# Kernel optimization log

Measured on AMD Instinct MI355X. Metric: run time of the kernel, lower is better.

The kernel has to match this reference:

```python
import jax, jax.numpy as jnp
import numpy as np

N, E, G = 50000, 800000, 512
F_IN, ED, NUM_CLASSES = 128, 3, 10
H1, C1, C2 = 4, 32, 64


def _add_self_loops(src, dst, eattr, n):
    # PyG add_self_loops with fill_value='mean': loop attr = mean of incoming edge attrs
    cnt = jax.ops.segment_sum(jnp.ones_like(dst, dtype=eattr.dtype), dst, num_segments=n)
    loop = jax.ops.segment_sum(eattr, dst, num_segments=n) / jnp.maximum(cnt, 1.0)[:, None]
    ar = jnp.arange(n)
    return (jnp.concatenate([src, ar]), jnp.concatenate([dst, ar]),
            jnp.concatenate([eattr, loop], axis=0))


def _gatv2(x, src, dst, eattr, Wl, bl, Wr, br, We, att, bias, heads, out_ch, concat, n):
    xl = (x @ Wl.T + bl).reshape(n, heads, out_ch)   # source transform (lin_l)
    xr = (x @ Wr.T + br).reshape(n, heads, out_ch)   # target transform (lin_r)
    ee = (eattr @ We.T).reshape(-1, heads, out_ch)   # edge transform (lin_edge, no bias)
    m = jax.nn.leaky_relu(xl[src] + xr[dst] + ee, 0.2)  # [E', H, C]
    score = jnp.einsum('ehc,hc->eh', m, att)
    # segment softmax over incoming edges of each target node
    smax = jax.ops.segment_max(score, dst, num_segments=n)
    ex = jnp.exp(score - smax[dst])
    denom = jax.ops.segment_sum(ex, dst, num_segments=n)
    alpha = ex / denom[dst]
    out = jax.ops.segment_sum(alpha[:, :, None] * xl[src], dst, num_segments=n)
    out = out.reshape(n, heads * out_ch) if concat else out.mean(axis=1)
    return out + bias


def setup_inputs() -> dict:
    key = jax.random.key(0)
    ks = jax.random.split(key, 24)
    s = 0.1
    return {
        'x': jax.random.normal(ks[0], (N, F_IN), jnp.float32),
        'edge_index': jax.random.randint(ks[1], (2, E), 0, N),
        'edge_attr': jax.random.normal(ks[2], (E, ED), jnp.float32),
        'batch': jnp.sort(jax.random.randint(ks[3], (N,), 0, G)),
        'u': jax.random.normal(ks[4], (G, 1), jnp.float32),
        'Wl1': jax.random.normal(ks[5], (H1 * C1, F_IN), jnp.float32) * s,
        'bl1': jnp.zeros((H1 * C1,), jnp.float32),
        'Wr1': jax.random.normal(ks[6], (H1 * C1, F_IN), jnp.float32) * s,
        'br1': jnp.zeros((H1 * C1,), jnp.float32),
        'We1': jax.random.normal(ks[7], (H1 * C1, ED), jnp.float32) * s,
        'att1': jax.random.normal(ks[8], (H1, C1), jnp.float32) * s,
        'b1': jnp.zeros((H1 * C1,), jnp.float32),
        'Wl2': jax.random.normal(ks[9], (C2, H1 * C1), jnp.float32) * s,
        'bl2': jnp.zeros((C2,), jnp.float32),
        'Wr2': jax.random.normal(ks[10], (C2, H1 * C1), jnp.float32) * s,
        'br2': jnp.zeros((C2,), jnp.float32),
        'We2': jax.random.normal(ks[11], (C2, ED), jnp.float32) * s,
        'att2': jax.random.normal(ks[12], (1, C2), jnp.float32) * s,
        'b2': jnp.zeros((C2,), jnp.float32),
        'W_lin1': jax.random.normal(ks[13], (32, 65), jnp.float32) * s,
        'b_lin1': jnp.zeros((32,), jnp.float32),
        'W_head': jax.random.normal(ks[14], (NUM_CLASSES, 32), jnp.float32) * s,
        'b_head': jnp.zeros((NUM_CLASSES,), jnp.float32),
    }


def reference(x, edge_index, edge_attr, batch, u,
              Wl1, bl1, Wr1, br1, We1, att1, b1,
              Wl2, bl2, Wr2, br2, We2, att2, b2,
              W_lin1, b_lin1, W_head, b_head):
    n = x.shape[0]
    src, dst, ea = _add_self_loops(edge_index[0], edge_index[1], edge_attr, n)
    h = jax.nn.elu(_gatv2(x, src, dst, ea, Wl1, bl1, Wr1, br1, We1, att1, b1, H1, C1, True, n))
    h = jax.nn.elu(_gatv2(h, src, dst, ea, Wl2, bl2, Wr2, br2, We2, att2, b2, 1, C2, False, n))
    cnt = jax.ops.segment_sum(jnp.ones((n,), h.dtype), batch, num_segments=G)
    pooled = jax.ops.segment_sum(h, batch, num_segments=G) / jnp.maximum(cnt, 1.0)[:, None]
    z = jax.nn.relu(jnp.concatenate([pooled, u], axis=1) @ W_lin1.T + b_lin1)
    return z @ W_head.T + b_head
```

## Files before the change

### kernel.cpp

```cpp
#include <hip/hip_runtime.h>
#include <hip/hip_fp16.h>
#include <math.h>


union H2U { __half2 h; unsigned u; };
typedef _Float16 hv2_t __attribute__((ext_vector_type(2)));
typedef unsigned uv4_t __attribute__((ext_vector_type(4)));

__device__ __forceinline__ __half2 hmax2(__half2 a, __half2 b) {
  union { __half2 h; hv2_t v; } x, y, r;
  x.h = a; y.h = b;
  r.v = __builtin_elementwise_max(x.v, y.v);
  return r.h;
}

#if __has_builtin(__builtin_amdgcn_fdot2)
__device__ __forceinline__ float dot2f(__half2 a, __half2 b, float c) {
  union { __half2 h; hv2_t v; } x, y;
  x.h = a; y.h = b;
  return __builtin_amdgcn_fdot2(x.v, y.v, c, false);
}
#else
__device__ __forceinline__ float dot2f(__half2 a, __half2 b, float c) {
  float2 af = __half22float2(a), bf = __half22float2(b);
  return fmaf(af.x, bf.x, fmaf(af.y, bf.y, c));
}
#endif

__global__ void hist_k(const int* __restrict__ dst, int* __restrict__ deg, int E) {
  int e = blockIdx.x * 256 + threadIdx.x;
  if (e < E) atomicAdd(&deg[dst[e]], 1);
}

__global__ void blocksum_k(const int* __restrict__ deg, int* __restrict__ bsum, int N) {
  __shared__ int s[256];
  int i = blockIdx.x * 256 + threadIdx.x;
  s[threadIdx.x] = (i < N) ? deg[i] : 0;
  __syncthreads();
  for (int off = 128; off; off >>= 1) {
    if (threadIdx.x < off) s[threadIdx.x] += s[threadIdx.x + off];
    __syncthreads();
  }
  if (threadIdx.x == 0) bsum[blockIdx.x] = s[0];
}

__global__ void scan_bsum_k(int* __restrict__ bsum, int nb) {
  __shared__ int s[256];
  int t = threadIdx.x;
  s[t] = (t < nb) ? bsum[t] : 0;
  __syncthreads();
  for (int off = 1; off < 256; off <<= 1) {
    int v = (t >= off) ? s[t - off] : 0;
    __syncthreads();
    if (t >= off) s[t] += v;
    __syncthreads();
  }
  int excl = (t == 0) ? 0 : s[t - 1];
  if (t < nb) bsum[t] = excl;
}

__global__ void writeptr_k(const int* __restrict__ deg, const int* __restrict__ bsum,
                           int* __restrict__ rowptr, int* __restrict__ cursor, int N, int E) {
  __shared__ int s[256];
  int t = threadIdx.x;
  int i = blockIdx.x * 256 + t;
  s[t] = (i < N) ? deg[i] : 0;
  __syncthreads();
  for (int off = 1; off < 256; off <<= 1) {
    int v = (t >= off) ? s[t - off] : 0;
    __syncthreads();
    if (t >= off) s[t] += v;
    __syncthreads();
  }
  int excl = bsum[blockIdx.x] + ((t == 0) ? 0 : s[t - 1]);
  if (i < N) {
    rowptr[i] = excl;
    cursor[i] = excl;
  }
  if (i == N - 1) rowptr[N] = E;
}

__global__ void fill_k(const int* __restrict__ src, const int* __restrict__ dst,
                       const float* __restrict__ eattr, int* __restrict__ cursor,
                       uint4* __restrict__ erec, int E) {
  int e = blockIdx.x * 256 + threadIdx.x;
  if (e >= E) return;
  int d = dst[e];
  int pos = atomicAdd(&cursor[d], 1);
  H2U a0, a1, a2;
  float e0 = eattr[e * 3 + 0], e1 = eattr[e * 3 + 1], e2 = eattr[e * 3 + 2];
  a0.h = __floats2half2_rn(e0, e0);
  a1.h = __floats2half2_rn(e1, e1);
  a2.h = __floats2half2_rn(e2, e2);
  uv4_t v = {(unsigned)src[e], a0.u, a1.u, a2.u};
  __builtin_nontemporal_store(v, (uv4_t*)&erec[pos]);
}

template <int J>
__global__ __launch_bounds__(256, 3) void node_linear2t_k(
    const float* __restrict__ X,
    const float* __restrict__ W1, const float* __restrict__ b1v,
    const float* __restrict__ W2, const float* __restrict__ b2v,
    __half* __restrict__ out1, float* __restrict__ out2, int nrows) {
  constexpr int K = 128, KB = 32;
  constexpr int JG = J / 4;
  constexpr int RG = 256 / JG;
  constexpr int RB = RG * 4;
  constexpr int XP2 = RB + 4;
  constexpr int WP2 = J + 4;
  __shared__ __align__(16) __half2 sXT2[K / 2][XP2];
  __shared__ __align__(16) __half2 sW1T2[KB / 2][WP2];
  __shared__ __align__(16) __half2 sW2T2[KB / 2][WP2];

  int tid = threadIdx.x;
  int n0 = blockIdx.x * RB;

  {
    int r = tid & (RB - 1);
    int kq0 = tid / RB;
    constexpr int KQS = 256 / RB;
    int n = n0 + r;
    bool ok = n < nrows;
    for (int kq = kq0; kq < K / 4; kq += KQS) {
      float4 v = ok ? *(const float4*)&X[(size_t)n * K + kq * 4]
                    : make_float4(0.f, 0.f, 0.f, 0.f);
      sXT2[kq * 2 + 0][r] = __floats2half2_rn(v.x, v.y);
      sXT2[kq * 2 + 1][r] = __floats2half2_rn(v.z, v.w);
    }
  }

  int jg = tid % JG;
  int rg = tid / JG;
  float acc1[4][4] = {}, acc2[4][4] = {};

  for (int kb = 0; kb < K / KB; ++kb) {
    __syncthreads();
    {
      int j = tid & (J - 1);
      int kq0 = tid / J;
      constexpr int KQS = 256 / J;
      for (int kq = kq0; kq < KB / 4; kq += KQS) {
        float4 v1 = *(const float4*)&W1[(size_t)j * K + kb * KB + kq * 4];
        float4 v2 = *(const float4*)&W2[(size_t)j * K + kb * KB + kq * 4];
        sW1T2[kq * 2 + 0][j] = __floats2half2_rn(v1.x, v1.y);
        sW1T2[kq * 2 + 1][j] = __floats2half2_rn(v1.z, v1.w);
        sW2T2[kq * 2 + 0][j] = __floats2half2_rn(v2.x, v2.y);
        sW2T2[kq * 2 + 1][j] = __floats2half2_rn(v2.z, v2.w);
      }
    }
    __syncthreads();
#pragma unroll
    for (int k2 = 0; k2 < KB / 2; ++k2) {
      const __half2* xp = &sXT2[kb * (KB / 2) + k2][rg * 4];
      const __half2* w1p = &sW1T2[k2][jg * 4];
      const __half2* w2p = &sW2T2[k2][jg * 4];
      __half2 xs2[4], w1s2[4], w2s2[4];
      *(float4*)xs2 = *(const float4*)xp;
      *(float4*)w1s2 = *(const float4*)w1p;
      *(float4*)w2s2 = *(const float4*)w2p;
#pragma unroll
      for (int i = 0; i < 4; ++i)
#pragma unroll
        for (int q = 0; q < 4; ++q) {
          acc1[i][q] = dot2f(xs2[i], w1s2[q], acc1[i][q]);
          acc2[i][q] = dot2f(xs2[i], w2s2[q], acc2[i][q]);
        }
    }
  }

  float4 bv1 = *(const float4*)&b1v[jg * 4];
  float4 bv2 = *(const float4*)&b2v[jg * 4];
#pragma unroll
  for (int i = 0; i < 4; ++i) {
    int n = n0 + rg * 4 + i;
    if (n < nrows) {
      H2U a, b;
      a.h = __floats2half2_rn(acc1[i][0] + bv1.x, acc1[i][1] + bv1.y);
      b.h = __floats2half2_rn(acc1[i][2] + bv1.z, acc1[i][3] + bv1.w);
      *(uint2*)&out1[(size_t)n * J + jg * 4] = make_uint2(a.u, b.u);
      float4 o2 = make_float4(acc2[i][0] + bv2.x, acc2[i][1] + bv2.y,
                              acc2[i][2] + bv2.z, acc2[i][3] + bv2.w);
      *(float4*)&out2[(size_t)n * J + jg * 4] = o2;
    }
  }
}

__global__ __launch_bounds__(256) void gat1_fused_k(
    const int* __restrict__ rowptr, const uint4* __restrict__ erec,
    const __half* __restrict__ xlh, const float* __restrict__ xr,
    const float* __restrict__ We, const float* __restrict__ att,
    const float* __restrict__ bias, float* __restrict__ out, int N) {
  constexpr int CH = 8;
  int lane = threadIdx.x & 63;
  int wave0 = __builtin_amdgcn_readfirstlane(
      (int)((blockIdx.x * 256 + threadIdx.x) >> 6));
  int nwaves = gridDim.x * 4;
  const __half2* xl2p = (const __half2*)xlh;
  int c0 = 2 * lane;
  __half2 w0p = __floats2half2_rn(We[c0 * 3 + 0], We[c0 * 3 + 3]);
  __half2 w1p = __floats2half2_rn(We[c0 * 3 + 1], We[c0 * 3 + 4]);
  __half2 w2p = __floats2half2_rn(We[c0 * 3 + 2], We[c0 * 3 + 5]);
  __half2 attp = __floats2half2_rn(att[c0], att[c0 + 1]);
  float2 attf = __half22float2(attp);
  float2 w0f = __half22float2(w0p), w1f = __half22float2(w1p), w2f = __half22float2(w2p);
  __half2 k02 = __floats2half2_rn(0.2f, 0.2f);
  float2 bv = make_float2(bias[c0], bias[c0 + 1]);

  for (int n = wave0; n < N; n += nwaves) {
    float2 xrv = *(const float2*)&xr[(size_t)n * 128 + c0];
    __half2 xrp = __floats2half2_rn(xrv.x, xrv.y);
    int beg = rowptr[n], end = rowptr[n + 1];
    int deg = end - beg;

    float acc0 = 0.f, acc1 = 0.f, den = 0.f;
    __half2 es0h = __floats2half2_rn(0.f, 0.f), es1h = es0h, es2h = es0h;

    int nfull = deg / CH;
    for (int ch = 0; ch < nfull; ++ch) {
      int b = beg + ch * CH;
      uint4 recs[CH];
#pragma unroll
      for (int j = 0; j < CH; ++j) recs[j] = erec[b + j];
      __half2 r_[CH];
#pragma unroll
      for (int j = 0; j < CH; ++j) {
        int s = __builtin_amdgcn_readfirstlane((int)recs[j].x);
        r_[j] = xl2p[(size_t)s * 64 + lane];
      }
#pragma unroll
      for (int j = 0; j < CH; ++j) {
        H2U e0, e1, e2;
        e0.u = recs[j].y; e1.u = recs[j].z; e2.u = recs[j].w;
        es0h = __hadd2(es0h, e0.h);
        es1h = __hadd2(es1h, e1.h);
        es2h = __hadd2(es2h, e2.h);
        __half2 m = __hadd2(r_[j], xrp);
        m = __hfma2(e0.h, w0p, m);
        m = __hfma2(e1.h, w1p, m);
        m = __hfma2(e2.h, w2p, m);
        m = hmax2(m, __hmul2(m, k02));
        float v = dot2f(m, attp, 0.f);
        v += __shfl_xor(v, 1);
        v += __shfl_xor(v, 2);
        v += __shfl_xor(v, 4);
        v += __shfl_xor(v, 8);
        float ex = __expf(v);
        float2 rfF = __half22float2(r_[j]);
        den += ex;
        acc0 = fmaf(ex, rfF.x, acc0);
        acc1 = fmaf(ex, rfF.y, acc1);
      }
    }
    {
      int b = beg + nfull * CH;
#pragma unroll
      for (int j = 0; j < CH; ++j) {
        int gi = b + j;
        bool valid = gi < end;
        uint4 rec = valid ? erec[gi] : make_uint4((unsigned)n, 0u, 0u, 0u);
        int s = __builtin_amdgcn_readfirstlane((int)rec.x);
        __half2 rf = xl2p[(size_t)s * 64 + lane];
        H2U e0, e1, e2;
        e0.u = rec.y; e1.u = rec.z; e2.u = rec.w;
        es0h = __hadd2(es0h, e0.h);
        es1h = __hadd2(es1h, e1.h);
        es2h = __hadd2(es2h, e2.h);
        __half2 m = __hadd2(rf, xrp);
        m = __hfma2(e0.h, w0p, m);
        m = __hfma2(e1.h, w1p, m);
        m = __hfma2(e2.h, w2p, m);
        m = hmax2(m, __hmul2(m, k02));
        float v = dot2f(m, attp, 0.f);
        v += __shfl_xor(v, 1);
        v += __shfl_xor(v, 2);
        v += __shfl_xor(v, 4);
        v += __shfl_xor(v, 8);
        float ex = valid ? __expf(v) : 0.f;
        float2 rfF = __half22float2(rf);
        den += ex;
        acc0 = fmaf(ex, rfF.x, acc0);
        acc1 = fmaf(ex, rfF.y, acc1);
      }
    }

    float invd = 1.0f / fmaxf((float)deg, 1.0f);
    float t0 = __half2float(__low2half(es0h)) * invd;
    float t1 = __half2float(__low2half(es1h)) * invd;
    float t2 = __half2float(__low2half(es2h)) * invd;
    float2 xls = __half22float2(xl2p[(size_t)n * 64 + lane]);
    float m0 = xls.x + xrv.x + t0 * w0f.x + t1 * w1f.x + t2 * w2f.x;
    float m1 = xls.y + xrv.y + t0 * w0f.y + t1 * w1f.y + t2 * w2f.y;
    m0 = fmaxf(m0, 0.2f * m0);
    m1 = fmaxf(m1, 0.2f * m1);
    float v = fmaf(m0, attf.x, m1 * attf.y);
    v += __shfl_xor(v, 1);
    v += __shfl_xor(v, 2);
    v += __shfl_xor(v, 4);
    v += __shfl_xor(v, 8);
    float ex = __expf(v);
    den += ex;
    acc0 = fmaf(ex, xls.x, acc0);
    acc1 = fmaf(ex, xls.y, acc1);

    float o0 = acc0 / den + bv.x;
    float o1 = acc1 / den + bv.y;
    o0 = o0 > 0.f ? o0 : __expf(o0) - 1.0f;
    o1 = o1 > 0.f ? o1 : __expf(o1) - 1.0f;
    *(float2*)&out[(size_t)n * 128 + c0] = make_float2(o0, o1);
  }
}

__global__ __launch_bounds__(256) void gat2_fused_k(
    const int* __restrict__ rowptr, const uint4* __restrict__ erec,
    const __half* __restrict__ xlh, const float* __restrict__ xr,
    const float* __restrict__ We, const float* __restrict__ att,
    const float* __restrict__ bias, float* __restrict__ out, int N) {
  constexpr int CP = 4;
  int lane = threadIdx.x & 63;
  int wave0 = __builtin_amdgcn_readfirstlane(
      (int)((blockIdx.x * 256 + threadIdx.x) >> 6));
  int nwaves = gridDim.x * 4;
  int sub = lane & 31, grp = lane >> 5;
  int c0 = 2 * sub;
  const __half2* xl2p = (const __half2*)xlh;
  __half2 w0p = __floats2half2_rn(We[c0 * 3 + 0], We[c0 * 3 + 3]);
  __half2 w1p = __floats2half2_rn(We[c0 * 3 + 1], We[c0 * 3 + 4]);
  __half2 w2p = __floats2half2_rn(We[c0 * 3 + 2], We[c0 * 3 + 5]);
  __half2 attp = __floats2half2_rn(att[c0], att[c0 + 1]);
  float2 attf = __half22float2(attp);
  float2 w0f = __half22float2(w0p), w1f = __half22float2(w1p), w2f = __half22float2(w2p);
  __half2 k02 = __floats2half2_rn(0.2f, 0.2f);
  float2 bv = make_float2(bias[c0], bias[c0 + 1]);

  for (int n = wave0; n < N; n += nwaves) {
    float2 xrv = *(const float2*)&xr[(size_t)n * 64 + c0];
    __half2 xrp = __floats2half2_rn(xrv.x, xrv.y);
    int beg = rowptr[n], end = rowptr[n + 1];
    int deg = end - beg;

    float acc0 = 0.f, acc1 = 0.f, den = 0.f;
    __half2 es0h = __floats2half2_rn(0.f, 0.f), es1h = es0h, es2h = es0h;

    int nfull = deg / (2 * CP);
    int b = beg + grp;
    for (int ch = 0; ch < nfull; ++ch) {
      uint4 recs[CP];
      __half2 r_[CP];
#pragma unroll
      for (int j = 0; j < CP; ++j) recs[j] = erec[b + 2 * j];
#pragma unroll
      for (int j = 0; j < CP; ++j) r_[j] = xl2p[(size_t)recs[j].x * 32 + sub];
#pragma unroll
      for (int j = 0; j < CP; ++j) {
        H2U e0, e1, e2;
        e0.u = recs[j].y; e1.u = recs[j].z; e2.u = recs[j].w;
        es0h = __hadd2(es0h, e0.h);
        es1h = __hadd2(es1h, e1.h);
        es2h = __hadd2(es2h, e2.h);
        __half2 m = __hadd2(r_[j], xrp);
        m = __hfma2(e0.h, w0p, m);
        m = __hfma2(e1.h, w1p, m);
        m = __hfma2(e2.h, w2p, m);
        m = hmax2(m, __hmul2(m, k02));
        float v = dot2f(m, attp, 0.f);
        v += __shfl_xor(v, 1);
        v += __shfl_xor(v, 2);
        v += __shfl_xor(v, 4);
        v += __shfl_xor(v, 8);
        v += __shfl_xor(v, 16);
        float ex = __expf(v);
        float2 rfF = __half22float2(r_[j]);
        den += ex;
        acc0 = fmaf(ex, rfF.x, acc0);
        acc1 = fmaf(ex, rfF.y, acc1);
      }
      b += 2 * CP;
    }
    {
      int tb = beg + nfull * 2 * CP;
#pragma unroll
      for (int j = 0; j < CP; ++j) {
        int gi = tb + 2 * j + grp;
        bool valid = gi < end;
        uint4 rec = valid ? erec[gi] : make_uint4((unsigned)n, 0u, 0u, 0u);
        __half2 rf = xl2p[(size_t)rec.x * 32 + sub];
        H2U e0, e1, e2;
        e0.u = rec.y; e1.u = rec.z; e2.u = rec.w;
        es0h = __hadd2(es0h, e0.h);
        es1h = __hadd2(es1h, e1.h);
        es2h = __hadd2(es2h, e2.h);
        __half2 m = __hadd2(rf, xrp);
        m = __hfma2(e0.h, w0p, m);
        m = __hfma2(e1.h, w1p, m);
        m = __hfma2(e2.h, w2p, m);
        m = hmax2(m, __hmul2(m, k02));
        float v = dot2f(m, attp, 0.f);
        v += __shfl_xor(v, 1);
        v += __shfl_xor(v, 2);
        v += __shfl_xor(v, 4);
        v += __shfl_xor(v, 8);
        v += __shfl_xor(v, 16);
        float ex = valid ? __expf(v) : 0.f;
        float2 rfF = __half22float2(rf);
        den += ex;
        acc0 = fmaf(ex, rfF.x, acc0);
        acc1 = fmaf(ex, rfF.y, acc1);
      }
    }

    float es0 = __half2float(__low2half(es0h));
    float es1 = __half2float(__low2half(es1h));
    float es2 = __half2float(__low2half(es2h));
    acc0 += __shfl_xor(acc0, 32);
    acc1 += __shfl_xor(acc1, 32);
    den += __shfl_xor(den, 32);
    es0 += __shfl_xor(es0, 32);
    es1 += __shfl_xor(es1, 32);
    es2 += __shfl_xor(es2, 32);

    float invd = 1.0f / fmaxf((float)deg, 1.0f);
    float t0 = es0 * invd, t1 = es1 * invd, t2 = es2 * invd;
    float2 xls = __half22float2(xl2p[(size_t)n * 32 + sub]);
    float m0 = xls.x + xrv.x + t0 * w0f.x + t1 * w1f.x + t2 * w2f.x;
    float m1 = xls.y + xrv.y + t0 * w0f.y + t1 * w1f.y + t2 * w2f.y;
    m0 = fmaxf(m0, 0.2f * m0);
    m1 = fmaxf(m1, 0.2f * m1);
    float v = fmaf(m0, attf.x, m1 * attf.y);
    v += __shfl_xor(v, 1);
    v += __shfl_xor(v, 2);
    v += __shfl_xor(v, 4);
    v += __shfl_xor(v, 8);
    v += __shfl_xor(v, 16);
    float ex = __expf(v);
    den += ex;
    acc0 = fmaf(ex, xls.x, acc0);
    acc1 = fmaf(ex, xls.y, acc1);

    if (grp == 0) {
      float o0 = acc0 / den + bv.x;
      float o1 = acc1 / den + bv.y;
      o0 = o0 > 0.f ? o0 : __expf(o0) - 1.0f;
      o1 = o1 > 0.f ? o1 : __expf(o1) - 1.0f;
      *(float2*)&out[(size_t)n * 64 + c0] = make_float2(o0, o1);
    }
  }
}

__global__ void final_mlp_k(const float* __restrict__ h2, const int* __restrict__ batch,
                            int N, const float* __restrict__ u,
                            const float* __restrict__ W1, const float* __restrict__ b1,
                            const float* __restrict__ Wh, const float* __restrict__ bh,
                            float* __restrict__ out) {
  __shared__ float comb[4][64];
  __shared__ float feat[65];
  __shared__ float z[32];
  int g = blockIdx.x;
  int t = threadIdx.x;
  int c = t & 63, q = t >> 6;
  int lo, hi;
  {
    int l = 0, h = N;
    while (l < h) { int m = (l + h) >> 1; if (batch[m] < g) l = m + 1; else h = m; }
    lo = l;
    h = N;
    while (l < h) { int m = (l + h) >> 1; if (batch[m] < g + 1) l = m + 1; else h = m; }
    hi = l;
  }
  float a = 0.f;
  for (int nn = lo + q; nn < hi; nn += 4) a += h2[(size_t)nn * 64 + c];
  comb[q][c] = a;
  __syncthreads();
  if (t < 64) {
    float s = comb[0][t] + comb[1][t] + comb[2][t] + comb[3][t];
    float inv = 1.0f / fmaxf((float)(hi - lo), 1.0f);
    feat[t] = s * inv;
    if (t == 0) feat[64] = u[g];
  }
  __syncthreads();
  if (t < 32) {
    float s = b1[t];
    for (int k = 0; k < 65; ++k) s += feat[k] * W1[t * 65 + k];
    z[t] = fmaxf(s, 0.0f);
  }
  __syncthreads();
  if (t < 10) {
    float s = bh[t];
    for (int k = 0; k < 32; ++k) s += z[k] * Wh[t * 32 + k];
    out[g * 10 + t] = s;
  }
}

extern "C" void kernel_launch(void* const* d_in, const int* in_sizes, int n_in,
                              void* d_out, int out_size, void* d_ws, size_t ws_size,
                              hipStream_t stream) {
  const float* x      = (const float*)d_in[0];
  const int*   eidx   = (const int*)d_in[1];
  const float* eattr  = (const float*)d_in[2];
  const int*   batch  = (const int*)d_in[3];
  const float* u      = (const float*)d_in[4];
  const float* Wl1    = (const float*)d_in[5];
  const float* bl1    = (const float*)d_in[6];
  const float* Wr1    = (const float*)d_in[7];
  const float* br1    = (const float*)d_in[8];
  const float* We1    = (const float*)d_in[9];
  const float* att1   = (const float*)d_in[10];
  const float* b1     = (const float*)d_in[11];
  const float* Wl2    = (const float*)d_in[12];
  const float* bl2    = (const float*)d_in[13];
  const float* Wr2    = (const float*)d_in[14];
  const float* br2    = (const float*)d_in[15];
  const float* We2    = (const float*)d_in[16];
  const float* att2   = (const float*)d_in[17];
  const float* b2     = (const float*)d_in[18];
  const float* W_lin1 = (const float*)d_in[19];
  const float* b_lin1 = (const float*)d_in[20];
  const float* W_head = (const float*)d_in[21];
  const float* b_head = (const float*)d_in[22];

  const int N = in_sizes[0] / 128;
  const int E = in_sizes[1] / 2;
  const int G = in_sizes[4];
  const int* srcp = eidx;
  const int* dstp = eidx + E;

  __half* bufh = (__half*)d_ws;
  float* buf2 = (float*)(bufh + (size_t)N * 128);
  float* buf3 = buf2 + (size_t)N * 128;
  uint4* erec = (uint4*)(buf3 + (size_t)N * 128);
  int* deg    = (int*)(erec + E);
  int* rowptr = deg + N;
  int* cursor = rowptr + N + 1;
  int* bsum   = cursor + N;

  const int nb = (N + 255) / 256;

  (void)hipMemsetAsync(deg, 0, sizeof(int) * (size_t)N, stream);
  hist_k<<<(E + 255) / 256, 256, 0, stream>>>(dstp, deg, E);
  blocksum_k<<<nb, 256, 0, stream>>>(deg, bsum, N);
  scan_bsum_k<<<1, 256, 0, stream>>>(bsum, nb);
  writeptr_k<<<nb, 256, 0, stream>>>(deg, bsum, rowptr, cursor, N, E);
  fill_k<<<(E + 255) / 256, 256, 0, stream>>>(srcp, dstp, eattr, cursor, erec, E);

  node_linear2t_k<128><<<(N + 31) / 32, 256, 0, stream>>>(x, Wl1, bl1, Wr1, br1,
                                                          bufh, buf2, N);
  gat1_fused_k<<<8192, 256, 0, stream>>>(rowptr, erec, bufh, buf2,
                                         We1, att1, b1, buf3, N);

  node_linear2t_k<64><<<(N + 63) / 64, 256, 0, stream>>>(buf3, Wl2, bl2, Wr2, br2,
                                                         bufh, buf2, N);
  gat2_fused_k<<<8192, 256, 0, stream>>>(rowptr, erec, bufh, buf2,
                                         We2, att2, b2, buf3, N);

  final_mlp_k<<<G, 256, 0, stream>>>(buf3, batch, N, u, W_lin1, b_lin1, W_head, b_head,
                                     (float*)d_out);
}
```

Measured before the change: 416.3 us.

## Materialize self-loop records in CSR and drop per-node self-loop epilogue

The edge histogram now records each edge's rank within its destination, so the fill kernel writes directly to rowptr+rank instead of using a second atomic cursor pass. The block-sum scan kernel is folded into writeptr, and rowptr reserves one extra slot per node for the self-loop. A new loopattr kernel computes the mean incoming edge attribute and writes a self-loop record, which removes the per-edge attribute accumulation and the separate self-loop epilogue from both GAT kernels. In exchange it adds a rank array, an extra kernel that rereads the edge records, and a redundant per-block reduction of the block sums.

```diff
diff --git a/kernel.cpp b/kernel.cpp
--- a/kernel.cpp
+++ b/kernel.cpp
@@ -27,9 +27,15 @@
 }
 #endif
 
-__global__ void hist_k(const int* __restrict__ dst, int* __restrict__ deg, int E) {
+__device__ __forceinline__ float lowf(unsigned u) {
+  H2U t; t.u = u;
+  return __half2float(__low2half(t.h));
+}
+
+__global__ void hist_k(const int* __restrict__ dst, int* __restrict__ deg,
+                       int* __restrict__ rank, int E) {
   int e = blockIdx.x * 256 + threadIdx.x;
-  if (e < E) atomicAdd(&deg[dst[e]], 1);
+  if (e < E) rank[e] = atomicAdd(&deg[dst[e]], 1);
 }
 
 __global__ void blocksum_k(const int* __restrict__ deg, int* __restrict__ bsum, int N) {
@@ -44,10 +50,20 @@
   if (threadIdx.x == 0) bsum[blockIdx.x] = s[0];
 }
 
-__global__ void scan_bsum_k(int* __restrict__ bsum, int nb) {
+__global__ void writeptr_k(const int* __restrict__ deg, const int* __restrict__ bsum,
+                           int* __restrict__ rowptr, int N, int E) {
   __shared__ int s[256];
+  __shared__ int bs[256];
   int t = threadIdx.x;
-  s[t] = (t < nb) ? bsum[t] : 0;
+  int i = blockIdx.x * 256 + t;
+  bs[t] = (t < (int)blockIdx.x) ? bsum[t] : 0;
+  s[t] = (i < N) ? deg[i] : 0;
+  __syncthreads();
+  for (int off = 128; off; off >>= 1) {
+    if (t < off) bs[t] += bs[t + off];
+    __syncthreads();
+  }
+  int base = bs[0];
   __syncthreads();
   for (int off = 1; off < 256; off <<= 1) {
     int v = (t >= off) ? s[t - off] : 0;
@@ -55,38 +71,17 @@
     if (t >= off) s[t] += v;
     __syncthreads();
   }
-  int excl = (t == 0) ? 0 : s[t - 1];
-  if (t < nb) bsum[t] = excl;
-}
-
-__global__ void writeptr_k(const int* __restrict__ deg, const int* __restrict__ bsum,
-                           int* __restrict__ rowptr, int* __restrict__ cursor, int N, int E) {
-  __shared__ int s[256];
-  int t = threadIdx.x;
-  int i = blockIdx.x * 256 + t;
-  s[t] = (i < N) ? deg[i] : 0;
-  __syncthreads();
-  for (int off = 1; off < 256; off <<= 1) {
-    int v = (t >= off) ? s[t - off] : 0;
-    __syncthreads();
-    if (t >= off) s[t] += v;
-    __syncthreads();
-  }
-  int excl = bsum[blockIdx.x] + ((t == 0) ? 0 : s[t - 1]);
-  if (i < N) {
-    rowptr[i] = excl;
-    cursor[i] = excl;
-  }
-  if (i == N - 1) rowptr[N] = E;
+  int excl = base + ((t == 0) ? 0 : s[t - 1]) + i;
+  if (i < N) rowptr[i] = excl;
+  if (i == N - 1) rowptr[N] = E + N;
 }
 
 __global__ void fill_k(const int* __restrict__ src, const int* __restrict__ dst,
-                       const float* __restrict__ eattr, int* __restrict__ cursor,
-                       uint4* __restrict__ erec, int E) {
+                       const float* __restrict__ eattr, const int* __restrict__ rowptr,
+                       const int* __restrict__ rank, uint4* __restrict__ erec, int E) {
   int e = blockIdx.x * 256 + threadIdx.x;
   if (e >= E) return;
-  int d = dst[e];
-  int pos = atomicAdd(&cursor[d], 1);
+  int pos = rowptr[dst[e]] + rank[e];
   H2U a0, a1, a2;
   float e0 = eattr[e * 3 + 0], e1 = eattr[e * 3 + 1], e2 = eattr[e * 3 + 2];
   a0.h = __floats2half2_rn(e0, e0);
@@ -94,6 +89,34 @@
   a2.h = __floats2half2_rn(e2, e2);
   uv4_t v = {(unsigned)src[e], a0.u, a1.u, a2.u};
   __builtin_nontemporal_store(v, (uv4_t*)&erec[pos]);
+}
+
+__global__ void loopattr_k(const int* __restrict__ rowptr, uint4* __restrict__ erec, int N) {
+  int lane = threadIdx.x & 63;
+  int n = (int)((blockIdx.x * 256 + threadIdx.x) >> 6);
+  if (n >= N) return;
+  int beg = rowptr[n], endr = rowptr[n + 1] - 1;
+  float f0 = 0.f, f1 = 0.f, f2 = 0.f;
+  for (int i = beg + lane; i < endr; i += 64) {
+    uint4 r = erec[i];
+    f0 += lowf(r.y);
+    f1 += lowf(r.z);
+    f2 += lowf(r.w);
+  }
+#pragma unroll
+  for (int off = 1; off < 64; off <<= 1) {
+    f0 += __shfl_xor(f0, off);
+    f1 += __shfl_xor(f1, off);
+    f2 += __shfl_xor(f2, off);
+  }
+  if (lane == 0) {
+    float inv = 1.0f / fmaxf((float)(endr - beg), 1.0f);
+    H2U a0, a1, a2;
+    a0.h = __floats2half2_rn(f0 * inv, f0 * inv);
+    a1.h = __floats2half2_rn(f1 * inv, f1 * inv);
+    a2.h = __floats2half2_rn(f2 * inv, f2 * inv);
+    erec[endr] = make_uint4((unsigned)n, a0.u, a1.u, a2.u);
+  }
 }
 
 template <int J>
@@ -201,8 +224,6 @@
   __half2 w1p = __floats2half2_rn(We[c0 * 3 + 1], We[c0 * 3 + 4]);
   __half2 w2p = __floats2half2_rn(We[c0 * 3 + 2], We[c0 * 3 + 5]);
   __half2 attp = __floats2half2_rn(att[c0], att[c0 + 1]);
-  float2 attf = __half22float2(attp);
-  float2 w0f = __half22float2(w0p), w1f = __half22float2(w1p), w2f = __half22float2(w2p);
   __half2 k02 = __floats2half2_rn(0.2f, 0.2f);
   float2 bv = make_float2(bias[c0], bias[c0 + 1]);
 
@@ -210,12 +231,11 @@
     float2 xrv = *(const float2*)&xr[(size_t)n * 128 + c0];
     __half2 xrp = __floats2half2_rn(xrv.x, xrv.y);
     int beg = rowptr[n], end = rowptr[n + 1];
-    int deg = end - beg;
+    int cnt = end - beg;
 
     float acc0 = 0.f, acc1 = 0.f, den = 0.f;
-    __half2 es0h = __floats2half2_rn(0.f, 0.f), es1h = es0h, es2h = es0h;
-
-    int nfull = deg / CH;
+
+    int nfull = cnt / CH;
     for (int ch = 0; ch < nfull; ++ch) {
       int b = beg + ch * CH;
       uint4 recs[CH];
@@ -231,9 +251,6 @@
       for (int j = 0; j < CH; ++j) {
         H2U e0, e1, e2;
         e0.u = recs[j].y; e1.u = recs[j].z; e2.u = recs[j].w;
-        es0h = __hadd2(es0h, e0.h);
-        es1h = __hadd2(es1h, e1.h);
-        es2h = __hadd2(es2h, e2.h);
         __half2 m = __hadd2(r_[j], xrp);
         m = __hfma2(e0.h, w0p, m);
         m = __hfma2(e1.h, w1p, m);
@@ -262,9 +279,6 @@
         __half2 rf = xl2p[(size_t)s * 64 + lane];
         H2U e0, e1, e2;
         e0.u = rec.y; e1.u = rec.z; e2.u = rec.w;
-        es0h = __hadd2(es0h, e0.h);
-        es1h = __hadd2(es1h, e1.h);
-        es2h = __hadd2(es2h, e2.h);
         __half2 m = __hadd2(rf, xrp);
         m = __hfma2(e0.h, w0p, m);
         m = __hfma2(e1.h, w1p, m);
@@ -282,25 +296,6 @@
         acc1 = fmaf(ex, rfF.y, acc1);
       }
     }
-
-    float invd = 1.0f / fmaxf((float)deg, 1.0f);
-    float t0 = __half2float(__low2half(es0h)) * invd;
-    float t1 = __half2float(__low2half(es1h)) * invd;
-    float t2 = __half2float(__low2half(es2h)) * invd;
-    float2 xls = __half22float2(xl2p[(size_t)n * 64 + lane]);
-    float m0 = xls.x + xrv.x + t0 * w0f.x + t1 * w1f.x + t2 * w2f.x;
-    float m1 = xls.y + xrv.y + t0 * w0f.y + t1 * w1f.y + t2 * w2f.y;
-    m0 = fmaxf(m0, 0.2f * m0);
-    m1 = fmaxf(m1, 0.2f * m1);
-    float v = fmaf(m0, attf.x, m1 * attf.y);
-    v += __shfl_xor(v, 1);
-    v += __shfl_xor(v, 2);
-    v += __shfl_xor(v, 4);
-    v += __shfl_xor(v, 8);
-    float ex = __expf(v);
-    den += ex;
-    acc0 = fmaf(ex, xls.x, acc0);
-    acc1 = fmaf(ex, xls.y, acc1);
 
     float o0 = acc0 / den + bv.x;
     float o1 = acc1 / den + bv.y;
@@ -327,8 +322,6 @@
   __half2 w1p = __floats2half2_rn(We[c0 * 3 + 1], We[c0 * 3 + 4]);
   __half2 w2p = __floats2half2_rn(We[c0 * 3 + 2], We[c0 * 3 + 5]);
   __half2 attp = __floats2half2_rn(att[c0], att[c0 + 1]);
-  float2 attf = __half22float2(attp);
-  float2 w0f = __half22float2(w0p), w1f = __half22float2(w1p), w2f = __half22float2(w2p);
   __half2 k02 = __floats2half2_rn(0.2f, 0.2f);
   float2 bv = make_float2(bias[c0], bias[c0 + 1]);
 
@@ -336,12 +329,11 @@
     float2 xrv = *(const float2*)&xr[(size_t)n * 64 + c0];
     __half2 xrp = __floats2half2_rn(xrv.x, xrv.y);
     int beg = rowptr[n], end = rowptr[n + 1];
-    int deg = end - beg;
+    int cnt = end - beg;
 
     float acc0 = 0.f, acc1 = 0.f, den = 0.f;
-    __half2 es0h = __floats2half2_rn(0.f, 0.f), es1h = es0h, es2h = es0h;
-
-    int nfull = deg / (2 * CP);
+
+    int nfull = cnt / (2 * CP);
     int b = beg + grp;
     for (int ch = 0; ch < nfull; ++ch) {
       uint4 recs[CP];
@@ -354,9 +346,6 @@
       for (int j = 0; j < CP; ++j) {
         H2U e0, e1, e2;
         e0.u = recs[j].y; e1.u = recs[j].z; e2.u = recs[j].w;
-        es0h = __hadd2(es0h, e0.h);
-        es1h = __hadd2(es1h, e1.h);
-        es2h = __hadd2(es2h, e2.h);
         __half2 m = __hadd2(r_[j], xrp);
         m = __hfma2(e0.h, w0p, m);
         m = __hfma2(e1.h, w1p, m);
@@ -386,9 +375,6 @@
         __half2 rf = xl2p[(size_t)rec.x * 32 + sub];
         H2U e0, e1, e2;
         e0.u = rec.y; e1.u = rec.z; e2.u = rec.w;
-        es0h = __hadd2(es0h, e0.h);
-        es1h = __hadd2(es1h, e1.h);
-        es2h = __hadd2(es2h, e2.h);
         __half2 m = __hadd2(rf, xrp);
         m = __hfma2(e0.h, w0p, m);
         m = __hfma2(e1.h, w1p, m);
@@ -408,33 +394,9 @@
       }
     }
 
-    float es0 = __half2float(__low2half(es0h));
-    float es1 = __half2float(__low2half(es1h));
-    float es2 = __half2float(__low2half(es2h));
     acc0 += __shfl_xor(acc0, 32);
     acc1 += __shfl_xor(acc1, 32);
     den += __shfl_xor(den, 32);
-    es0 += __shfl_xor(es0, 32);
-    es1 += __shfl_xor(es1, 32);
-    es2 += __shfl_xor(es2, 32);
-
-    float invd = 1.0f / fmaxf((float)deg, 1.0f);
-    float t0 = es0 * invd, t1 = es1 * invd, t2 = es2 * invd;
-    float2 xls = __half22float2(xl2p[(size_t)n * 32 + sub]);
-    float m0 = xls.x + xrv.x + t0 * w0f.x + t1 * w1f.x + t2 * w2f.x;
-    float m1 = xls.y + xrv.y + t0 * w0f.y + t1 * w1f.y + t2 * w2f.y;
-    m0 = fmaxf(m0, 0.2f * m0);
-    m1 = fmaxf(m1, 0.2f * m1);
-    float v = fmaf(m0, attf.x, m1 * attf.y);
-    v += __shfl_xor(v, 1);
-    v += __shfl_xor(v, 2);
-    v += __shfl_xor(v, 4);
-    v += __shfl_xor(v, 8);
-    v += __shfl_xor(v, 16);
-    float ex = __expf(v);
-    den += ex;
-    acc0 = fmaf(ex, xls.x, acc0);
-    acc1 = fmaf(ex, xls.y, acc1);
 
     if (grp == 0) {
       float o0 = acc0 / den + bv.x;
@@ -527,19 +489,19 @@
   float* buf2 = (float*)(bufh + (size_t)N * 128);
   float* buf3 = buf2 + (size_t)N * 128;
   uint4* erec = (uint4*)(buf3 + (size_t)N * 128);
-  int* deg    = (int*)(erec + E);
+  int* rank   = (int*)(erec + ((size_t)E + N));
+  int* deg    = rank + E;
   int* rowptr = deg + N;
-  int* cursor = rowptr + N + 1;
-  int* bsum   = cursor + N;
+  int* bsum   = rowptr + N + 1;
 
   const int nb = (N + 255) / 256;
 
   (void)hipMemsetAsync(deg, 0, sizeof(int) * (size_t)N, stream);
-  hist_k<<<(E + 255) / 256, 256, 0, stream>>>(dstp, deg, E);
+  hist_k<<<(E + 255) / 256, 256, 0, stream>>>(dstp, deg, rank, E);
   blocksum_k<<<nb, 256, 0, stream>>>(deg, bsum, N);
-  scan_bsum_k<<<1, 256, 0, stream>>>(bsum, nb);
-  writeptr_k<<<nb, 256, 0, stream>>>(deg, bsum, rowptr, cursor, N, E);
-  fill_k<<<(E + 255) / 256, 256, 0, stream>>>(srcp, dstp, eattr, cursor, erec, E);
+  writeptr_k<<<nb, 256, 0, stream>>>(deg, bsum, rowptr, N, E);
+  fill_k<<<(E + 255) / 256, 256, 0, stream>>>(srcp, dstp, eattr, rowptr, rank, erec, E);
+  loopattr_k<<<(N * 64 + 255) / 256, 256, 0, stream>>>(rowptr, erec, N);
 
   node_linear2t_k<128><<<(N + 31) / 32, 256, 0, stream>>>(x, Wl1, bl1, Wr1, br1,
                                                           bufh, buf2, N);
```

Result: faster. 394.8 us (-5.2%).
